# Kernel optimization log

Measured on AMD Instinct MI355X. Metric: run time of the kernel, lower is better.

Reference implementation:

```python
import jax, jax.numpy as jnp
import numpy as np

N_NODES = 100000
N_EDGES = 1600000
D = 128
NUM_GRAPHS = 256


def setup_inputs() -> dict:
    key = jax.random.key(0)
    ks = jax.random.split(key, 8)
    x = jax.random.normal(ks[0], (N_NODES, D), dtype=jnp.float32)
    edge_index = jax.random.randint(ks[1], (2, N_EDGES), 0, N_NODES, dtype=jnp.int32)
    edge_attr = jax.random.normal(ks[2], (N_EDGES, D), dtype=jnp.float32) * 0.1
    batch = jnp.sort(jax.random.randint(ks[3], (N_NODES,), 0, NUM_GRAPHS, dtype=jnp.int32))
    primary = jax.random.randint(ks[4], (N_NODES,), 0, 2, dtype=jnp.int32)  # 1=primary, 0=condition
    scale = 1.0 / np.sqrt(D)
    W1 = jax.random.normal(ks[5], (D, D), dtype=jnp.float32) * scale
    b1 = jnp.zeros((D,), dtype=jnp.float32)
    W2 = jax.random.normal(ks[6], (D, D), dtype=jnp.float32) * scale
    b2 = jnp.zeros((D,), dtype=jnp.float32)
    return {"x": x, "edge_index": edge_index, "edge_attr": edge_attr,
            "batch": batch, "primary": primary,
            "W1": W1, "b1": b1, "W2": W2, "b2": b2}


def reference(x, edge_index, edge_attr, batch, primary, W1, b1, W2, b2):
    n = x.shape[0]
    # --- GIN-style GNN layer: node_rep = MLP(x + sum_{e:(s->d)} (x[s] + e_attr)) ---
    src, dst = edge_index[0], edge_index[1]
    msg = x[src] + edge_attr                                  # [E, D] gather (memory-bound)
    agg = jax.ops.segment_sum(msg, dst, num_segments=n)       # [N, D] scatter-add
    h = jax.nn.relu((x + agg) @ W1 + b1) @ W2 + b2            # [N, D]

    # --- per-graph mean pool over condition nodes (primary == 0) ---
    cond = (primary == 0)
    condf = cond.astype(h.dtype)[:, None]
    csum = jax.ops.segment_sum(h * condf, batch, num_segments=NUM_GRAPHS)   # [G, D]
    ccnt = jax.ops.segment_sum(condf, batch, num_segments=NUM_GRAPHS)       # [G, 1]
    # graphs with no condition nodes get a zero pool (matches torch branch)
    pool = jnp.where(ccnt > 0, csum / jnp.maximum(ccnt, 1.0), 0.0)          # [G, D]

    # --- assemble rows: per graph, primary rows [h | cond_pool] first, then zero rows
    # for condition nodes (matches the torch concat order) ---
    key = batch * 2 + cond.astype(batch.dtype)      # primary nodes sort before condition nodes
    order = jnp.argsort(key, stable=True)
    h_o = h[order]                                   # [N, D]
    pool_o = pool[batch[order]]                      # [N, D]
    prim_o = (primary[order] == 1)[:, None]
    out = jnp.where(prim_o, jnp.concatenate([h_o, pool_o], axis=1), 0.0)    # [N, 2D]
    return out
```

## Files before the change

### kernel.cpp

```cpp
#include <hip/hip_runtime.h>

#define D 128
#define NG 256

typedef __attribute__((ext_vector_type(8))) short bf16x8;
typedef __attribute__((ext_vector_type(4))) float f32x4;
typedef __attribute__((ext_vector_type(4))) float f4;
typedef __attribute__((ext_vector_type(2))) int i2;
typedef __attribute__((ext_vector_type(4))) ushort u16x4;

__device__ inline ushort f2bf(float f) {
  uint b = __float_as_uint(f);
  return (ushort)((b + 0x7fffu + ((b >> 16) & 1u)) >> 16);
}
__device__ inline float bf2f(ushort u) { return __uint_as_float((uint)u << 16); }

__global__ __launch_bounds__(256) void deg_counts_kernel(const int* __restrict__ ei,
                                                         int* __restrict__ deg,
                                                         const int* __restrict__ batch,
                                                         const int* __restrict__ primary,
                                                         int* __restrict__ ncount,
                                                         int* __restrict__ ccnt, int E, int N) {
  int e = blockIdx.x * blockDim.x + threadIdx.x;
  if (e < E) {
    int d = ei[E + e];
    atomicAdd(&deg[d], 1);
  }
  if (e < N) {
    int g = batch[e];
    atomicAdd(&ncount[g], 1);
    if (primary[e] == 0) atomicAdd(&ccnt[g], 1);
  }
}

__global__ __launch_bounds__(256) void scan_block_sums(const int* __restrict__ deg,
                                                       int* __restrict__ bsum, int N) {
  __shared__ int red[256];
  int t = threadIdx.x;
  int base = blockIdx.x * 1024;
  int s = 0;
#pragma unroll
  for (int j = 0; j < 4; ++j) {
    int i = base + t * 4 + j;
    if (i < N) s += deg[i];
  }
  red[t] = s;
  __syncthreads();
  for (int o = 128; o > 0; o >>= 1) {
    if (t < o) red[t] += red[t + o];
    __syncthreads();
  }
  if (t == 0) bsum[blockIdx.x] = red[0];
}

__global__ void scan_bsum(int* __restrict__ bsum, int nb) {
  if (threadIdx.x == 0) {
    int run = 0;
    for (int i = 0; i < nb; ++i) {
      int v = bsum[i];
      bsum[i] = run;
      run += v;
    }
  }
}

__global__ __launch_bounds__(256) void scan_final(const int* __restrict__ deg,
                                                  const int* __restrict__ bsum,
                                                  int* __restrict__ off, int N) {
  __shared__ int ts[256];
  int t = threadIdx.x;
  int base = blockIdx.x * 1024;
  int v[4];
  int s = 0;
#pragma unroll
  for (int j = 0; j < 4; ++j) {
    int i = base + t * 4 + j;
    v[j] = (i < N) ? deg[i] : 0;
    s += v[j];
  }
  ts[t] = s;
  __syncthreads();
  for (int o = 1; o < 256; o <<= 1) {
    int u = (t >= o) ? ts[t - o] : 0;
    __syncthreads();
    ts[t] += u;
    __syncthreads();
  }
  int excl = ts[t] - s + bsum[blockIdx.x];
#pragma unroll
  for (int j = 0; j < 4; ++j) {
    int i = base + t * 4 + j;
    if (i < N) off[i] = excl;
    excl += v[j];
    if (i == N - 1) off[N] = excl;
  }
}

__global__ __launch_bounds__(256) void fill_kernel(const int* __restrict__ ei,
                                                   const int* __restrict__ off,
                                                   int* __restrict__ cursor,
                                                   i2* __restrict__ csr, int E) {
  int e = blockIdx.x * blockDim.x + threadIdx.x;
  if (e >= E) return;
  int s = ei[e];
  int d = ei[E + e];
  int slot = atomicAdd(&cursor[d], 1);
  i2 v;
  v.x = s;
  v.y = e;
  csr[off[d] + slot] = v;
}

__global__ __launch_bounds__(256) void cvt_kernel(const float* __restrict__ x,
                                                  ushort* __restrict__ xb,
                                                  const float* __restrict__ W1,
                                                  const float* __restrict__ W2,
                                                  ushort* __restrict__ W1T,
                                                  ushort* __restrict__ W2T, int total4) {
  int i = blockIdx.x * blockDim.x + threadIdx.x;
  if (i < total4) {
    f4 v = __builtin_nontemporal_load(&((const f4*)x)[i]);
    u16x4 o;
    o.x = f2bf(v.x);
    o.y = f2bf(v.y);
    o.z = f2bf(v.z);
    o.w = f2bf(v.w);
    ((u16x4*)xb)[i] = o;
  }
  if (i < 2 * D * D) {
    int w = i >> 14;
    int k = (i >> 7) & 127;
    int n = i & 127;
    const float* src = w ? W2 : W1;
    ushort* dst = w ? W2T : W1T;
    dst[n * 128 + k] = f2bf(src[k * 128 + n]);
  }
}

__global__ void scan_kernel(const int* __restrict__ ncount, int* __restrict__ gstart) {
  __shared__ int a[NG];
  int tx = threadIdx.x;
  int v = ncount[tx];
  a[tx] = v;
  __syncthreads();
  for (int off = 1; off < NG; off <<= 1) {
    int u = (tx >= off) ? a[tx - off] : 0;
    __syncthreads();
    a[tx] += u;
    __syncthreads();
  }
  gstart[tx] = a[tx] - v;
  if (tx == NG - 1) gstart[NG] = a[tx];
}

__global__ __launch_bounds__(256) void rank_kernel(const int* __restrict__ primary,
                                                   const int* __restrict__ gstart,
                                                   const int* __restrict__ ccnt,
                                                   int* __restrict__ pos) {
  int g = blockIdx.x;
  int s = gstart[g], e = gstart[g + 1];
  int pcnt = (e - s) - ccnt[g];
  __shared__ int wcntP[4], wcntC[4];
  int prun = 0, crun = 0;
  for (int i0 = s; i0 < e; i0 += 256) {
    int n = i0 + threadIdx.x;
    bool valid = n < e;
    int isP = (valid && primary[n] == 1) ? 1 : 0;
    int isC = (valid && primary[n] != 1) ? 1 : 0;
    unsigned long long mP = __ballot(isP);
    unsigned long long mC = __ballot(isC);
    int lane = threadIdx.x & 63;
    int wid = threadIdx.x >> 6;
    if (lane == 0) { wcntP[wid] = __popcll(mP); wcntC[wid] = __popcll(mC); }
    __syncthreads();
    int preP = __popcll(mP & ((1ULL << lane) - 1ULL));
    int preC = __popcll(mC & ((1ULL << lane) - 1ULL));
    int woffP = 0, woffC = 0;
#pragma unroll
    for (int ww = 0; ww < 4; ++ww)
      if (ww < wid) { woffP += wcntP[ww]; woffC += wcntC[ww]; }
    int totP = wcntP[0] + wcntP[1] + wcntP[2] + wcntP[3];
    int totC = wcntC[0] + wcntC[1] + wcntC[2] + wcntC[3];
    if (valid) {
      if (isP)
        pos[n] = s + prun + woffP + preP;
      else
        pos[n] = ~(s + pcnt + crun + woffC + preC);
    }
    prun += totP;
    crun += totC;
    __syncthreads();
  }
}

__global__ __launch_bounds__(256, 4) void fused_gather_mlp_kernel(
    const ushort* __restrict__ xb, const float* __restrict__ ea,
    const i2* __restrict__ csr, const int* __restrict__ off, float* __restrict__ out,
    const ushort* __restrict__ W1T, const float* __restrict__ b1,
    const ushort* __restrict__ W2T, const float* __restrict__ b2,
    const int* __restrict__ batch, const int* __restrict__ primary,
    const int* __restrict__ pos, float* __restrict__ csum, int N) {
  __shared__ ushort ylds[64][D];
  __shared__ ushort tl[4][16][D];
  __shared__ float csl[4][D];
  const int tid = threadIdx.x;
  const int base = blockIdx.x * 64;

  for (int i = tid; i < 4 * D; i += 256) ((float*)csl)[i] = 0.f;
  const int gmin = batch[base < N ? base : N - 1];

  {
    const int gid = tid >> 5;
    const int c = tid & 31;
    const f4* ea4 = (const f4*)ea;
    const u16x4* xb4 = (const u16x4*)xb;
    for (int i = 0; i < 8; ++i) {
      const int m = gid * 8 + i;
      const int n = base + m;
      f4 acc = {0.f, 0.f, 0.f, 0.f};
      if (n < N) {
        u16x4 self = xb4[(size_t)n * 32 + c];
        acc.x = bf2f(self.x);
        acc.y = bf2f(self.y);
        acc.z = bf2f(self.z);
        acc.w = bf2f(self.w);
        int s = off[n], e = off[n + 1];
        int k = s;
        for (; k + 4 <= e; k += 4) {
          i2 p0 = csr[k];
          i2 p1 = csr[k + 1];
          i2 p2 = csr[k + 2];
          i2 p3 = csr[k + 3];
          f4 a0 = __builtin_nontemporal_load(&ea4[(size_t)p0.y * 32 + c]);
          f4 a1 = __builtin_nontemporal_load(&ea4[(size_t)p1.y * 32 + c]);
          f4 a2 = __builtin_nontemporal_load(&ea4[(size_t)p2.y * 32 + c]);
          f4 a3 = __builtin_nontemporal_load(&ea4[(size_t)p3.y * 32 + c]);
          u16x4 u0 = xb4[(size_t)p0.x * 32 + c];
          u16x4 u1 = xb4[(size_t)p1.x * 32 + c];
          u16x4 u2 = xb4[(size_t)p2.x * 32 + c];
          u16x4 u3 = xb4[(size_t)p3.x * 32 + c];
          acc.x += (a0.x + bf2f(u0.x)) + (a1.x + bf2f(u1.x));
          acc.y += (a0.y + bf2f(u0.y)) + (a1.y + bf2f(u1.y));
          acc.z += (a0.z + bf2f(u0.z)) + (a1.z + bf2f(u1.z));
          acc.w += (a0.w + bf2f(u0.w)) + (a1.w + bf2f(u1.w));
          acc.x += (a2.x + bf2f(u2.x)) + (a3.x + bf2f(u3.x));
          acc.y += (a2.y + bf2f(u2.y)) + (a3.y + bf2f(u3.y));
          acc.z += (a2.z + bf2f(u2.z)) + (a3.z + bf2f(u3.z));
          acc.w += (a2.w + bf2f(u2.w)) + (a3.w + bf2f(u3.w));
        }
        for (; k < e; ++k) {
          i2 p0 = csr[k];
          f4 a0 = __builtin_nontemporal_load(&ea4[(size_t)p0.y * 32 + c]);
          u16x4 u0 = xb4[(size_t)p0.x * 32 + c];
          acc.x += a0.x + bf2f(u0.x);
          acc.y += a0.y + bf2f(u0.y);
          acc.z += a0.z + bf2f(u0.z);
          acc.w += a0.w + bf2f(u0.w);
        }
      }
      u16x4 o;
      o.x = f2bf(acc.x);
      o.y = f2bf(acc.y);
      o.z = f2bf(acc.z);
      o.w = f2bf(acc.w);
      *(u16x4*)((char*)&ylds[m][0] + ((c * 8) ^ (i << 4))) = o;
    }
  }
  __syncthreads();

  const int w = tid >> 6;
  const int l = tid & 63;
  const int lr = l & 15;
  const int lg = l >> 4;
  const int m0 = base + w * 16;

  f32x4 acc[8];
#pragma unroll
  for (int t = 0; t < 8; ++t) {
    float bv = b1[t * 16 + lr];
    acc[t][0] = bv; acc[t][1] = bv; acc[t][2] = bv; acc[t][3] = bv;
  }
  const char* arow_base = (const char*)&ylds[w * 16 + lr][0];
  const int arow_swz = (lr & 7) << 4;
#pragma unroll
  for (int kk = 0; kk < 4; ++kk) {
    bf16x8 a = *(const bf16x8*)(arow_base + ((kk * 64 + lg * 16) ^ arow_swz));
#pragma unroll
    for (int t = 0; t < 8; ++t) {
      bf16x8 b = *(const bf16x8*)&W1T[(size_t)(t * 16 + lr) * D + kk * 32 + lg * 8];
      acc[t] = __builtin_amdgcn_mfma_f32_16x16x32_bf16(a, b, acc[t], 0, 0, 0);
    }
  }
#pragma unroll
  for (int t = 0; t < 8; ++t) {
#pragma unroll
    for (int r = 0; r < 4; ++r) {
      float v = acc[t][r];
      v = v > 0.f ? v : 0.f;
      int m = lg * 4 + r;
      int col = (t * 16 + lr) ^ ((m & 7) << 3);
      tl[w][m][col] = f2bf(v);
    }
  }
  __syncthreads();

  f32x4 acc2[8];
#pragma unroll
  for (int t = 0; t < 8; ++t) {
    float bv = b2[t * 16 + lr];
    acc2[t][0] = bv; acc2[t][1] = bv; acc2[t][2] = bv; acc2[t][3] = bv;
  }
#pragma unroll
  for (int kk = 0; kk < 4; ++kk) {
    bf16x8 a = *(const bf16x8*)&tl[w][lr][(kk * 32 + lg * 8) ^ ((lr & 7) << 3)];
#pragma unroll
    for (int t = 0; t < 8; ++t) {
      bf16x8 b = *(const bf16x8*)&W2T[(size_t)(t * 16 + lr) * D + kk * 32 + lg * 8];
      acc2[t] = __builtin_amdgcn_mfma_f32_16x16x32_bf16(a, b, acc2[t], 0, 0, 0);
    }
  }

#pragma unroll
  for (int r = 0; r < 4; ++r) {
    int m = m0 + lg * 4 + r;
    if (m >= N) continue;
    int p = pos[m];
    if (p >= 0) {
      size_t ro = (size_t)p * 256;
#pragma unroll
      for (int t = 0; t < 8; ++t)
        __builtin_nontemporal_store(acc2[t][r], &out[ro + t * 16 + lr]);
    } else {
      size_t ro = (size_t)(~p) * 256;
#pragma unroll
      for (int t = 0; t < 8; ++t) {
        __builtin_nontemporal_store(0.0f, &out[ro + t * 16 + lr]);
        __builtin_nontemporal_store(0.0f, &out[ro + 128 + t * 16 + lr]);
      }
      int g = batch[m];
      int gl = g - gmin;
      if (gl < 4) {
#pragma unroll
        for (int t = 0; t < 8; ++t) atomicAdd(&csl[gl][t * 16 + lr], acc2[t][r]);
      } else {
#pragma unroll
        for (int t = 0; t < 8; ++t)
          unsafeAtomicAdd(&csum[(size_t)g * D + t * 16 + lr], acc2[t][r]);
      }
    }
  }
  __syncthreads();
  for (int i = tid; i < 4 * D; i += 256) {
    float v = ((float*)csl)[i];
    if (v != 0.f) {
      int gl = i >> 7, c = i & 127;
      unsafeAtomicAdd(&csum[(size_t)(gmin + gl) * D + c], v);
    }
  }
}

__global__ __launch_bounds__(256) void poolwrite_kernel(const float* __restrict__ csum,
                                                        const int* __restrict__ ccnt,
                                                        const int* __restrict__ batch,
                                                        const int* __restrict__ pos,
                                                        float* __restrict__ out, int N) {
  long long tid = (long long)blockIdx.x * blockDim.x + threadIdx.x;
  int n = (int)(tid >> 5);
  int c = (int)(tid & 31);
  if (n >= N) return;
  int p = pos[n];
  if (p < 0) return;
  int g = batch[n];
  int cnt = ccnt[g];
  f4 v = {0.f, 0.f, 0.f, 0.f};
  if (cnt > 0) {
    f4 s4 = ((const f4*)csum)[(size_t)g * 32 + c];
    float inv = 1.0f / (float)cnt;
    v = s4 * inv;
  }
  __builtin_nontemporal_store(v, &((f4*)out)[(size_t)p * 64 + 32 + c]);
}

extern "C" void kernel_launch(void* const* d_in, const int* in_sizes, int n_in,
                              void* d_out, int out_size, void* d_ws, size_t ws_size,
                              hipStream_t stream) {
  const float* x = (const float*)d_in[0];
  const int* ei = (const int*)d_in[1];
  const float* ea = (const float*)d_in[2];
  const int* batch = (const int*)d_in[3];
  const int* primary = (const int*)d_in[4];
  const float* W1 = (const float*)d_in[5];
  const float* b1 = (const float*)d_in[6];
  const float* W2 = (const float*)d_in[7];
  const float* b2 = (const float*)d_in[8];
  float* out = (float*)d_out;

  const int N = in_sizes[0] / D;
  const int E = in_sizes[1] / 2;
  const int nb = (N + 1023) / 1024;

  float* csum = (float*)d_ws;
  ushort* xb = (ushort*)(csum + (size_t)NG * D);
  ushort* W1T = xb + (size_t)N * D;
  ushort* W2T = W1T + D * D;
  i2* csr = (i2*)(W2T + D * D);
  int* ip = (int*)(csr + (size_t)E);
  int* deg = ip;
  int* off = deg + N;
  int* cursor = off + N + 4;
  int* bsum = cursor + N;
  int* ccnt = bsum + 128;
  int* ncount = ccnt + NG;
  int* gstart = ncount + NG;
  int* pos = gstart + 260;

  hipMemsetAsync(csum, 0, (size_t)NG * D * 4, stream);
  hipMemsetAsync(deg, 0, (size_t)N * 4, stream);
  hipMemsetAsync(cursor, 0, (size_t)N * 4, stream);
  hipMemsetAsync(ccnt, 0, (size_t)NG * 2 * 4, stream);

  deg_counts_kernel<<<(E + 255) / 256, 256, 0, stream>>>(ei, deg, batch, primary, ncount, ccnt,
                                                         E, N);
  scan_block_sums<<<nb, 256, 0, stream>>>(deg, bsum, N);
  scan_bsum<<<1, 64, 0, stream>>>(bsum, nb);
  scan_final<<<nb, 256, 0, stream>>>(deg, bsum, off, N);
  fill_kernel<<<(E + 255) / 256, 256, 0, stream>>>(ei, off, cursor, csr, E);
  cvt_kernel<<<((N * D / 4) + 255) / 256, 256, 0, stream>>>(x, xb, W1, W2, W1T, W2T, N * D / 4);
  scan_kernel<<<1, NG, 0, stream>>>(ncount, gstart);
  rank_kernel<<<NG, 256, 0, stream>>>(primary, gstart, ccnt, pos);
  fused_gather_mlp_kernel<<<(N + 63) / 64, 256, 0, stream>>>(xb, ea, csr, off, out, W1T, b1,
                                                             W2T, b2, batch, primary, pos,
                                                             csum, N);
  poolwrite_kernel<<<(int)(((long long)N * 32 + 255) / 256), 256, 0, stream>>>(csum, ccnt, batch,
                                                                               pos, out, N);
}
```

Baseline: 632.3 us.

## Materialize bf16 edge messages in dst-sorted order before the reduce-MLP

Replaces the CSR fill plus random edge_attr gather with a per-edge kernel that computes x[src]+edge_attr in bf16 and writes it straight into a dst-sorted message buffer. The reduce kernel then streams contiguous message rows instead of chasing edge indices. It also merges degree counting with the x and weight bf16 conversion, and parallelises the block-sum scan. The cost is an extra write and read of an E×D bf16 buffer, a much larger workspace, and an added bf16 rounding of each message.

```diff
diff --git a/kernel.cpp b/kernel.cpp
--- a/kernel.cpp
+++ b/kernel.cpp
@@ -6,7 +6,6 @@
 typedef __attribute__((ext_vector_type(8))) short bf16x8;
 typedef __attribute__((ext_vector_type(4))) float f32x4;
 typedef __attribute__((ext_vector_type(4))) float f4;
-typedef __attribute__((ext_vector_type(2))) int i2;
 typedef __attribute__((ext_vector_type(4))) ushort u16x4;
 
 __device__ inline ushort f2bf(float f) {
@@ -15,21 +14,33 @@
 }
 __device__ inline float bf2f(ushort u) { return __uint_as_float((uint)u << 16); }
 
-__global__ __launch_bounds__(256) void deg_counts_kernel(const int* __restrict__ ei,
-                                                         int* __restrict__ deg,
-                                                         const int* __restrict__ batch,
-                                                         const int* __restrict__ primary,
-                                                         int* __restrict__ ncount,
-                                                         int* __restrict__ ccnt, int E, int N) {
-  int e = blockIdx.x * blockDim.x + threadIdx.x;
-  if (e < E) {
-    int d = ei[E + e];
-    atomicAdd(&deg[d], 1);
-  }
-  if (e < N) {
-    int g = batch[e];
+__global__ __launch_bounds__(256) void prep_kernel(
+    const int* __restrict__ ei, int* __restrict__ deg,
+    const int* __restrict__ batch, const int* __restrict__ primary,
+    int* __restrict__ ncount, int* __restrict__ ccnt,
+    const float* __restrict__ x, ushort* __restrict__ xb,
+    const float* __restrict__ W1, const float* __restrict__ W2,
+    ushort* __restrict__ W1T, ushort* __restrict__ W2T, int E, int N, int total4) {
+  int i = blockIdx.x * blockDim.x + threadIdx.x;
+  if (i < E) atomicAdd(&deg[ei[E + i]], 1);
+  if (i < N) {
+    int g = batch[i];
     atomicAdd(&ncount[g], 1);
-    if (primary[e] == 0) atomicAdd(&ccnt[g], 1);
+    if (primary[i] == 0) atomicAdd(&ccnt[g], 1);
+  }
+  if (i < total4) {
+    f4 v = __builtin_nontemporal_load(&((const f4*)x)[i]);
+    u16x4 o;
+    o.x = f2bf(v.x); o.y = f2bf(v.y); o.z = f2bf(v.z); o.w = f2bf(v.w);
+    ((u16x4*)xb)[i] = o;
+  }
+  if (i < 2 * D * D) {
+    int w = i >> 14;
+    int k = (i >> 7) & 127;
+    int n = i & 127;
+    const float* src = w ? W2 : W1;
+    ushort* dst = w ? W2T : W1T;
+    dst[n * 128 + k] = f2bf(src[k * 128 + n]);
   }
 }
 
@@ -54,14 +65,18 @@
 }
 
 __global__ void scan_bsum(int* __restrict__ bsum, int nb) {
-  if (threadIdx.x == 0) {
-    int run = 0;
-    for (int i = 0; i < nb; ++i) {
-      int v = bsum[i];
-      bsum[i] = run;
-      run += v;
-    }
-  }
+  __shared__ int a[128];
+  int t = threadIdx.x;
+  int v = (t < nb) ? bsum[t] : 0;
+  a[t] = v;
+  __syncthreads();
+  for (int o = 1; o < 128; o <<= 1) {
+    int u = (t >= o) ? a[t - o] : 0;
+    __syncthreads();
+    a[t] += u;
+    __syncthreads();
+  }
+  if (t < nb) bsum[t] = a[t] - v;
 }
 
 __global__ __launch_bounds__(256) void scan_final(const int* __restrict__ deg,
@@ -96,45 +111,27 @@
   }
 }
 
-__global__ __launch_bounds__(256) void fill_kernel(const int* __restrict__ ei,
-                                                   const int* __restrict__ off,
-                                                   int* __restrict__ cursor,
-                                                   i2* __restrict__ csr, int E) {
-  int e = blockIdx.x * blockDim.x + threadIdx.x;
-  if (e >= E) return;
-  int s = ei[e];
-  int d = ei[E + e];
-  int slot = atomicAdd(&cursor[d], 1);
-  i2 v;
-  v.x = s;
-  v.y = e;
-  csr[off[d] + slot] = v;
-}
-
-__global__ __launch_bounds__(256) void cvt_kernel(const float* __restrict__ x,
-                                                  ushort* __restrict__ xb,
-                                                  const float* __restrict__ W1,
-                                                  const float* __restrict__ W2,
-                                                  ushort* __restrict__ W1T,
-                                                  ushort* __restrict__ W2T, int total4) {
-  int i = blockIdx.x * blockDim.x + threadIdx.x;
-  if (i < total4) {
-    f4 v = __builtin_nontemporal_load(&((const f4*)x)[i]);
-    u16x4 o;
-    o.x = f2bf(v.x);
-    o.y = f2bf(v.y);
-    o.z = f2bf(v.z);
-    o.w = f2bf(v.w);
-    ((u16x4*)xb)[i] = o;
-  }
-  if (i < 2 * D * D) {
-    int w = i >> 14;
-    int k = (i >> 7) & 127;
-    int n = i & 127;
-    const float* src = w ? W2 : W1;
-    ushort* dst = w ? W2T : W1T;
-    dst[n * 128 + k] = f2bf(src[k * 128 + n]);
-  }
+__global__ __launch_bounds__(256, 8) void msg_build_kernel(
+    const int* __restrict__ ei, const ushort* __restrict__ xb,
+    const float* __restrict__ ea, const int* __restrict__ off,
+    int* __restrict__ cursor, ushort* __restrict__ msg, int E) {
+  int g = (int)(((long long)blockIdx.x * 256 + threadIdx.x) >> 5);
+  int c = threadIdx.x & 31;
+  if (g >= E) return;
+  int s = ei[g];
+  int d = ei[E + g];
+  int slot;
+  if (c == 0) slot = atomicAdd(&cursor[d], 1);
+  slot = __shfl(slot, 0, 32);
+  long long row = (long long)off[d] + slot;
+  f4 a = __builtin_nontemporal_load(&((const f4*)ea)[(size_t)g * 32 + c]);
+  u16x4 u = ((const u16x4*)xb)[(size_t)s * 32 + c];
+  u16x4 o;
+  o.x = f2bf(a.x + bf2f(u.x));
+  o.y = f2bf(a.y + bf2f(u.y));
+  o.z = f2bf(a.z + bf2f(u.z));
+  o.w = f2bf(a.w + bf2f(u.w));
+  __builtin_nontemporal_store(o, &((u16x4*)msg)[(size_t)row * 32 + c]);
 }
 
 __global__ void scan_kernel(const int* __restrict__ ncount, int* __restrict__ gstart) {
@@ -193,9 +190,9 @@
   }
 }
 
-__global__ __launch_bounds__(256, 4) void fused_gather_mlp_kernel(
-    const ushort* __restrict__ xb, const float* __restrict__ ea,
-    const i2* __restrict__ csr, const int* __restrict__ off, float* __restrict__ out,
+__global__ __launch_bounds__(256, 4) void fused_reduce_mlp_kernel(
+    const ushort* __restrict__ xb, const ushort* __restrict__ msg,
+    const int* __restrict__ off, float* __restrict__ out,
     const ushort* __restrict__ W1T, const float* __restrict__ b1,
     const ushort* __restrict__ W2T, const float* __restrict__ b2,
     const int* __restrict__ batch, const int* __restrict__ primary,
@@ -212,7 +209,7 @@
   {
     const int gid = tid >> 5;
     const int c = tid & 31;
-    const f4* ea4 = (const f4*)ea;
+    const u16x4* msg4 = (const u16x4*)msg;
     const u16x4* xb4 = (const u16x4*)xb;
     for (int i = 0; i < 8; ++i) {
       const int m = gid * 8 + i;
@@ -224,38 +221,28 @@
         acc.y = bf2f(self.y);
         acc.z = bf2f(self.z);
         acc.w = bf2f(self.w);
-        int s = off[n], e = off[n + 1];
-        int k = s;
+        int k = off[n];
+        const int e = off[n + 1];
         for (; k + 4 <= e; k += 4) {
-          i2 p0 = csr[k];
-          i2 p1 = csr[k + 1];
-          i2 p2 = csr[k + 2];
-          i2 p3 = csr[k + 3];
-          f4 a0 = __builtin_nontemporal_load(&ea4[(size_t)p0.y * 32 + c]);
-          f4 a1 = __builtin_nontemporal_load(&ea4[(size_t)p1.y * 32 + c]);
-          f4 a2 = __builtin_nontemporal_load(&ea4[(size_t)p2.y * 32 + c]);
-          f4 a3 = __builtin_nontemporal_load(&ea4[(size_t)p3.y * 32 + c]);
-          u16x4 u0 = xb4[(size_t)p0.x * 32 + c];
-          u16x4 u1 = xb4[(size_t)p1.x * 32 + c];
-          u16x4 u2 = xb4[(size_t)p2.x * 32 + c];
-          u16x4 u3 = xb4[(size_t)p3.x * 32 + c];
-          acc.x += (a0.x + bf2f(u0.x)) + (a1.x + bf2f(u1.x));
-          acc.y += (a0.y + bf2f(u0.y)) + (a1.y + bf2f(u1.y));
-          acc.z += (a0.z + bf2f(u0.z)) + (a1.z + bf2f(u1.z));
-          acc.w += (a0.w + bf2f(u0.w)) + (a1.w + bf2f(u1.w));
-          acc.x += (a2.x + bf2f(u2.x)) + (a3.x + bf2f(u3.x));
-          acc.y += (a2.y + bf2f(u2.y)) + (a3.y + bf2f(u3.y));
-          acc.z += (a2.z + bf2f(u2.z)) + (a3.z + bf2f(u3.z));
-          acc.w += (a2.w + bf2f(u2.w)) + (a3.w + bf2f(u3.w));
+          u16x4 u0 = msg4[(size_t)k * 32 + c];
+          u16x4 u1 = msg4[(size_t)(k + 1) * 32 + c];
+          u16x4 u2 = msg4[(size_t)(k + 2) * 32 + c];
+          u16x4 u3 = msg4[(size_t)(k + 3) * 32 + c];
+          acc.x += bf2f(u0.x) + bf2f(u1.x);
+          acc.y += bf2f(u0.y) + bf2f(u1.y);
+          acc.z += bf2f(u0.z) + bf2f(u1.z);
+          acc.w += bf2f(u0.w) + bf2f(u1.w);
+          acc.x += bf2f(u2.x) + bf2f(u3.x);
+          acc.y += bf2f(u2.y) + bf2f(u3.y);
+          acc.z += bf2f(u2.z) + bf2f(u3.z);
+          acc.w += bf2f(u2.w) + bf2f(u3.w);
         }
         for (; k < e; ++k) {
-          i2 p0 = csr[k];
-          f4 a0 = __builtin_nontemporal_load(&ea4[(size_t)p0.y * 32 + c]);
-          u16x4 u0 = xb4[(size_t)p0.x * 32 + c];
-          acc.x += a0.x + bf2f(u0.x);
-          acc.y += a0.y + bf2f(u0.y);
-          acc.z += a0.z + bf2f(u0.z);
-          acc.w += a0.w + bf2f(u0.w);
+          u16x4 u0 = msg4[(size_t)k * 32 + c];
+          acc.x += bf2f(u0.x);
+          acc.y += bf2f(u0.y);
+          acc.z += bf2f(u0.z);
+          acc.w += bf2f(u0.w);
         }
       }
       u16x4 o;
@@ -398,13 +385,14 @@
   const int N = in_sizes[0] / D;
   const int E = in_sizes[1] / 2;
   const int nb = (N + 1023) / 1024;
+  const int total4 = N * D / 4;
 
   float* csum = (float*)d_ws;
   ushort* xb = (ushort*)(csum + (size_t)NG * D);
   ushort* W1T = xb + (size_t)N * D;
   ushort* W2T = W1T + D * D;
-  i2* csr = (i2*)(W2T + D * D);
-  int* ip = (int*)(csr + (size_t)E);
+  ushort* msg = W2T + D * D;
+  int* ip = (int*)(msg + (size_t)E * D);
   int* deg = ip;
   int* off = deg + N;
   int* cursor = off + N + 4;
@@ -419,18 +407,20 @@
   hipMemsetAsync(cursor, 0, (size_t)N * 4, stream);
   hipMemsetAsync(ccnt, 0, (size_t)NG * 2 * 4, stream);
 
-  deg_counts_kernel<<<(E + 255) / 256, 256, 0, stream>>>(ei, deg, batch, primary, ncount, ccnt,
-                                                         E, N);
+  prep_kernel<<<(total4 + 255) / 256, 256, 0, stream>>>(ei, deg, batch, primary, ncount, ccnt,
+                                                        x, xb, W1, W2, W1T, W2T, E, N, total4);
   scan_block_sums<<<nb, 256, 0, stream>>>(deg, bsum, N);
-  scan_bsum<<<1, 64, 0, stream>>>(bsum, nb);
+  scan_bsum<<<1, 128, 0, stream>>>(bsum, nb);
   scan_final<<<nb, 256, 0, stream>>>(deg, bsum, off, N);
-  fill_kernel<<<(E + 255) / 256, 256, 0, stream>>>(ei, off, cursor, csr, E);
-  cvt_kernel<<<((N * D / 4) + 255) / 256, 256, 0, stream>>>(x, xb, W1, W2, W1T, W2T, N * D / 4);
   scan_kernel<<<1, NG, 0, stream>>>(ncount, gstart);
   rank_kernel<<<NG, 256, 0, stream>>>(primary, gstart, ccnt, pos);
-  fused_gather_mlp_kernel<<<(N + 63) / 64, 256, 0, stream>>>(xb, ea, csr, off, out, W1T, b1,
-                                                             W2T, b2, batch, primary, pos,
-                                                             csum, N);
+  {
+    long long threads = (long long)E * 32;
+    msg_build_kernel<<<(int)((threads + 255) / 256), 256, 0, stream>>>(ei, xb, ea, off, cursor,
+                                                                       msg, E);
+  }
+  fused_reduce_mlp_kernel<<<(N + 63) / 64, 256, 0, stream>>>(xb, msg, off, out, W1T, b1, W2T,
+                                                             b2, batch, primary, pos, csum, N);
   poolwrite_kernel<<<(int)(((long long)N * 32 + 255) / 256), 256, 0, stream>>>(csum, ccnt, batch,
                                                                                pos, out, N);
 }
```

After: 701.8 us. +11.0%, slower.
